# Kernel tuning notes

Measured on AMD Instinct MI355X. Metric: run time of the kernel, lower is better.

## Reference

```python
import jax, jax.numpy as jnp
import numpy as np
import math

HIDDEN = 256

def setup_inputs() -> dict:
    key = jax.random.key(0)
    ks = jax.random.split(key, 4)
    x = jax.random.normal(ks[0], (64, 1024, 32), dtype=jnp.float32)
    Wq = jax.random.normal(ks[1], (32, HIDDEN), dtype=jnp.float32) * (1.0 / math.sqrt(32))
    Wk = jax.random.normal(ks[2], (32, HIDDEN), dtype=jnp.float32) * (1.0 / math.sqrt(32))
    Wv = jax.random.normal(ks[3], (32, HIDDEN), dtype=jnp.float32) * (1.0 / math.sqrt(32))
    bq = jnp.zeros((HIDDEN,), jnp.float32)
    bk = jnp.zeros((HIDDEN,), jnp.float32)
    bv = jnp.zeros((HIDDEN,), jnp.float32)
    return {"x": x, "Wq": Wq, "bq": bq, "Wk": Wk, "bk": bk, "Wv": Wv, "bv": bv}

def reference(x, Wq, bq, Wk, bk, Wv, bv):
    # per-sample single-head attention; softmax FIRST, then divide by sqrt(hidden)
    Q = jnp.einsum('bsi,ih->bsh', x, Wq) + bq  # [B,S,H]
    K = jnp.einsum('bsi,ih->bsh', x, Wk) + bk
    V = jnp.einsum('bsi,ih->bsh', x, Wv) + bv
    scores = jnp.einsum('bqh,bkh->bqk', Q, K)  # [B,S,S]
    attn = jax.nn.softmax(scores, axis=-1) / jnp.sqrt(jnp.float32(Q.shape[-1]))
    Z = jnp.einsum('bqk,bkh->bqh', attn, V)
    return Z
```

## Files before the change

kernel.cpp:

```cpp
#include <hip/hip_runtime.h>
#include <math.h>

#define NB   64
#define SEQ  1024
#define DIN  32
#define HID  256
#define QT   128
#define KT   64
#define NKT  (SEQ/KT)

typedef float        f32x16 __attribute__((ext_vector_type(16)));
typedef short        s16x8  __attribute__((ext_vector_type(8)));
typedef unsigned int u32x4v __attribute__((ext_vector_type(4)));
typedef unsigned int u32x2v __attribute__((ext_vector_type(2)));

#define MFMA32(A,B,C) __builtin_amdgcn_mfma_f32_32x32x16_bf16(A,B,C,0,0,0)

#define SETB(g,p) (((g)*2+(p))*12288)
#define ATS_OFF   49152
#define SMEM_SZ   (ATS_OFF + 4224)

__device__ __forceinline__ unsigned pk_bf16(float lo, float hi) {
  unsigned r;
  asm("v_cvt_pk_bf16_f32 %0, %1, %2" : "=v"(r) : "v"(lo), "v"(hi));
  return r;
}
__device__ __forceinline__ void plswap(unsigned &vdst, unsigned &vsrc) {
  u32x2v r = __builtin_amdgcn_permlane32_swap(vdst, vsrc, false, false);
  vdst = r[0]; vsrc = r[1];
}
__device__ __forceinline__ float cross_max(float v) {
  u32x2v r = __builtin_amdgcn_permlane32_swap(__float_as_uint(v), __float_as_uint(v), false, false);
  return fmaxf(__uint_as_float(r[0]), __uint_as_float(r[1]));
}
__device__ __forceinline__ float cross_add(float v) {
  u32x2v r = __builtin_amdgcn_permlane32_swap(__float_as_uint(v), __float_as_uint(v), false, false);
  return __uint_as_float(r[0]) + __uint_as_float(r[1]);
}
__device__ __forceinline__ s16x8 frag4(unsigned a, unsigned b, unsigned c, unsigned d) {
  u32x4v t; t[0]=a; t[1]=b; t[2]=c; t[3]=d;
  return __builtin_bit_cast(s16x8, t);
}
__device__ __forceinline__ unsigned bf16_hi_bits(float f) {
  unsigned ux = __float_as_uint(f);
  return (ux + 0x7fffu + ((ux >> 16) & 1u)) >> 16;
}

__global__ void precompute_kernel(const float* __restrict__ Wq, const float* __restrict__ Wk,
                                  const float* __restrict__ bq, const float* __restrict__ Wv,
                                  float* __restrict__ ws) {
  const int gid = blockIdx.x * 256 + threadIdx.x;
  if (gid < 1024) {
    int i = gid >> 5, j = gid & 31;
    const float* a  = Wq + j * HID;
    const float* b2 = Wk + i * HID;
    float a0 = 0.f, a1 = 0.f, a2 = 0.f, a3 = 0.f;
    for (int h = 0; h < HID; h += 8) {
      float4 x1 = *(const float4*)(a + h);
      float4 y1 = *(const float4*)(b2 + h);
      float4 x2 = *(const float4*)(a + h + 4);
      float4 y2 = *(const float4*)(b2 + h + 4);
      a0 = fmaf(x1.x, y1.x, a0); a1 = fmaf(x1.y, y1.y, a1);
      a2 = fmaf(x1.z, y1.z, a2); a3 = fmaf(x1.w, y1.w, a3);
      a0 = fmaf(x2.x, y2.x, a0); a1 = fmaf(x2.y, y2.y, a1);
      a2 = fmaf(x2.z, y2.z, a2); a3 = fmaf(x2.w, y2.w, a3);
    }
    ws[gid] = (a0 + a1) + (a2 + a3);
  } else if (gid < 1056) {
    int i2 = gid - 1024;
    const float* b2 = Wk + i2 * HID;
    float acc = 0.f;
    for (int h = 0; h < HID; ++h) acc = fmaf(b2[h], bq[h], acc);
    ws[1024 + i2] = acc;
  } else if (gid < 1056 + HID * 16) {
    int e = gid - 1056;
    int h = e >> 4, d = e & 15;
    ((unsigned*)((char*)ws + 4224))[e] = pk_bf16(Wv[(2*d) * HID + h], Wv[(2*d+1) * HID + h]);
  }
}

__global__ __launch_bounds__(512, 4) void attn_kernel(
    const float* __restrict__ x, const float* __restrict__ ws,
    const float* __restrict__ bv, float* __restrict__ out) {
  __shared__ __align__(16) char smem[SMEM_SZ];
  const int b    = blockIdx.y;
  const int q0   = blockIdx.x * QT;
  const int t    = threadIdx.x;
  const int grp  = t >> 8;
  const int ts   = t & 255;
  const int wid  = t >> 6;
  const int wq   = wid & 3;
  const int lane = t & 63;
  const int w    = lane >> 5;
  const int lq   = lane & 31;
  const float* xb = x + (size_t)b * SEQ * DIN;

  float* ATs = (float*)(smem + ATS_OFF);
  for (int e = t; e < 1056; e += 512) ATs[e] = ws[e];

  {
    const int sb = SETB(grp, 0);
    const int r = ts >> 2, s4 = ts & 3;
    const float* src = xb + (size_t)(grp * KT + r) * DIN + s4 * 8;
    float4 va = *(const float4*)src;
    float4 vb = *(const float4*)(src + 4);
    unsigned h0 = bf16_hi_bits(va.x) | (bf16_hi_bits(va.y) << 16);
    unsigned h1 = bf16_hi_bits(va.z) | (bf16_hi_bits(va.w) << 16);
    unsigned h2 = bf16_hi_bits(vb.x) | (bf16_hi_bits(vb.y) << 16);
    unsigned h3 = bf16_hi_bits(vb.z) | (bf16_hi_bits(vb.w) << 16);
    unsigned l0 = bf16_hi_bits(va.x - __uint_as_float(h0<<16)) | (bf16_hi_bits(va.y - __uint_as_float(h0 & 0xffff0000u)) << 16);
    unsigned l1 = bf16_hi_bits(va.z - __uint_as_float(h1<<16)) | (bf16_hi_bits(va.w - __uint_as_float(h1 & 0xffff0000u)) << 16);
    unsigned l2 = bf16_hi_bits(vb.x - __uint_as_float(h2<<16)) | (bf16_hi_bits(vb.y - __uint_as_float(h2 & 0xffff0000u)) << 16);
    unsigned l3 = bf16_hi_bits(vb.z - __uint_as_float(h3<<16)) | (bf16_hi_bits(vb.w - __uint_as_float(h3 & 0xffff0000u)) << 16);
    int off = r*64 + ((s4 ^ (r & 3)) << 4);
    *(u32x4v*)(smem + sb + off)        = (u32x4v){h0,h1,h2,h3};
    *(u32x4v*)(smem + sb + 4096 + off) = (u32x4v){l0,l1,l2,l3};
    const int ci = ts & 31, cr = (ts >> 5) * 8;
    const float* cs = xb + (size_t)(grp * KT + cr) * DIN + ci;
    float c0=cs[0], c1=cs[DIN], c2=cs[2*DIN], c3=cs[3*DIN];
    float c4=cs[4*DIN], c5=cs[5*DIN], c6=cs[6*DIN], c7=cs[7*DIN];
    unsigned t0 = pk_bf16(c0,c1), t1 = pk_bf16(c2,c3), t2 = pk_bf16(c4,c5), t3 = pk_bf16(c6,c7);
    int toff = sb + 8192 + ci*128 + (((ts>>5) ^ (ci & 7)) << 4);
    *(u32x4v*)(smem + toff) = (u32x4v){t0,t1,t2,t3};
  }
  __syncthreads();

  float g[16];
  {
    float xq[32];
    const float* xrow = xb + (size_t)(q0 + wq*32 + lq) * DIN;
    #pragma unroll
    for (int c = 0; c < 8; ++c) {
      float4 v = *(const float4*)(xrow + c*4);
      xq[c*4+0]=v.x; xq[c*4+1]=v.y; xq[c*4+2]=v.z; xq[c*4+3]=v.w;
    }
    #pragma unroll
    for (int ii = 0; ii < 16; ++ii) {
      const int i = 8*w + 16*(ii>>3) + (ii&7);
      const float* ar = ATs + i*32;
      float acc = ATs[1024 + i];
      #pragma unroll
      for (int j = 0; j < 8; ++j) {
        float4 av = *(const float4*)(ar + j*4);
        acc = fmaf(xq[j*4+0], av.x, acc);
        acc = fmaf(xq[j*4+1], av.y, acc);
        acc = fmaf(xq[j*4+2], av.z, acc);
        acc = fmaf(xq[j*4+3], av.w, acc);
      }
      g[ii] = acc;
    }
  }
  s16x8 G0h, G0l, G1h, G1l;
  {
    unsigned gh[2][4], gl[2][4];
    #pragma unroll
    for (int Ks = 0; Ks < 2; ++Ks)
      #pragma unroll
      for (int d = 0; d < 4; ++d) {
        float ga = g[Ks*8 + 2*d], gb = g[Ks*8 + 2*d + 1];
        unsigned hp = bf16_hi_bits(ga) | (bf16_hi_bits(gb) << 16);
        unsigned lp = bf16_hi_bits(ga - __uint_as_float(hp<<16)) |
                      (bf16_hi_bits(gb - __uint_as_float(hp & 0xffff0000u)) << 16);
        gh[Ks][d] = hp; gl[Ks][d] = lp;
      }
    G0h = frag4(gh[0][0],gh[0][1],gh[0][2],gh[0][3]);
    G0l = frag4(gl[0][0],gl[0][1],gl[0][2],gl[0][3]);
    G1h = frag4(gh[1][0],gh[1][1],gh[1][2],gh[1][3]);
    G1l = frag4(gl[1][0],gl[1][1],gl[1][2],gl[1][3]);
  }

  f32x16 oacc;
  #pragma unroll
  for (int r = 0; r < 16; ++r) oacc[r] = 0.f;
  float m = -INFINITY, l = 0.f;

  for (int j = 0; j < NKT/2; ++j) {
    const bool hn = (j + 1 < NKT/2);
    float4 va, vb;
    float c0=0,c1=0,c2=0,c3=0,c4=0,c5=0,c6=0,c7=0;
    if (hn) {
      const int ktn = 2*(j+1) + grp;
      const int r = ts >> 2, s4 = ts & 3;
      const float* src = xb + (size_t)(ktn*KT + r) * DIN + s4*8;
      va = *(const float4*)src;
      vb = *(const float4*)(src + 4);
      const int ci = ts & 31, cr = (ts >> 5) * 8;
      const float* cs = xb + (size_t)(ktn*KT + cr) * DIN + ci;
      c0=cs[0]; c1=cs[DIN]; c2=cs[2*DIN]; c3=cs[3*DIN];
      c4=cs[4*DIN]; c5=cs[5*DIN]; c6=cs[6*DIN]; c7=cs[7*DIN];
    }

    const int sb = SETB(grp, j & 1);
    const char* bh = smem + sb;
    const char* bl = smem + sb + 4096;
    const int co0 = ((w    ) ^ (lq & 3)) << 4;
    const int co1 = ((w + 2) ^ (lq & 3)) << 4;
    s16x8 ah00 = *(const s16x8*)(bh + lq*64 + co0);
    s16x8 ah01 = *(const s16x8*)(bh + lq*64 + co1);
    s16x8 al00 = *(const s16x8*)(bl + lq*64 + co0);
    s16x8 al01 = *(const s16x8*)(bl + lq*64 + co1);
    s16x8 ah10 = *(const s16x8*)(bh + (32+lq)*64 + co0);
    s16x8 ah11 = *(const s16x8*)(bh + (32+lq)*64 + co1);
    s16x8 al10 = *(const s16x8*)(bl + (32+lq)*64 + co0);
    s16x8 al11 = *(const s16x8*)(bl + (32+lq)*64 + co1);
    f32x16 sa0, sa1;
    #pragma unroll
    for (int r = 0; r < 16; ++r) { sa0[r] = 0.f; sa1[r] = 0.f; }
    sa0 = MFMA32(ah00, G0h, sa0); sa0 = MFMA32(ah00, G0l, sa0); sa0 = MFMA32(al00, G0h, sa0);
    sa0 = MFMA32(ah01, G1h, sa0); sa0 = MFMA32(ah01, G1l, sa0); sa0 = MFMA32(al01, G1h, sa0);
    sa1 = MFMA32(ah10, G0h, sa1); sa1 = MFMA32(ah10, G0l, sa1); sa1 = MFMA32(al10, G0h, sa1);
    sa1 = MFMA32(ah11, G1h, sa1); sa1 = MFMA32(ah11, G1l, sa1); sa1 = MFMA32(al11, G1h, sa1);

    float tm = sa0[0];
    #pragma unroll
    for (int r = 1; r < 16; ++r) tm = fmaxf(tm, sa0[r]);
    #pragma unroll
    for (int r = 0; r < 16; ++r) tm = fmaxf(tm, sa1[r]);
    tm = cross_max(tm);
    float mn = fmaxf(m, tm);
    float alpha = __expf(m - mn);
    m = mn;
    float ps = 0.f;
    #pragma unroll
    for (int r = 0; r < 16; ++r) { float p = __expf(sa0[r] - mn); sa0[r] = p; ps += p; }
    #pragma unroll
    for (int r = 0; r < 16; ++r) { float p = __expf(sa1[r] - mn); sa1[r] = p; ps += p; }
    ps = cross_add(ps);
    l = l * alpha + ps;
    #pragma unroll
    for (int r = 0; r < 16; ++r) oacc[r] *= alpha;

    const char* bt = smem + sb + 8192;
    {
      unsigned u0 = pk_bf16(sa0[0], sa0[1]),  u1 = pk_bf16(sa0[2], sa0[3]);
      unsigned v0 = pk_bf16(sa0[4], sa0[5]),  v1 = pk_bf16(sa0[6], sa0[7]);
      plswap(u0, v0); plswap(u1, v1);
      s16x8 at0 = *(const s16x8*)(bt + lq*128 + (((0 + w) ^ (lq & 7)) << 4));
      oacc = MFMA32(at0, frag4(u0, u1, v0, v1), oacc);

      unsigned u2 = pk_bf16(sa0[8], sa0[9]),   u3 = pk_bf16(sa0[10], sa0[11]);
      unsigned v2 = pk_bf16(sa0[12], sa0[13]), v3 = pk_bf16(sa0[14], sa0[15]);
      plswap(u2, v2); plswap(u3, v3);
      s16x8 at1 = *(const s16x8*)(bt + lq*128 + (((2 + w) ^ (lq & 7)) << 4));
      oacc = MFMA32(at1, frag4(u2, u3, v2, v3), oacc);

      unsigned u4 = pk_bf16(sa1[0], sa1[1]),  u5 = pk_bf16(sa1[2], sa1[3]);
      unsigned v4 = pk_bf16(sa1[4], sa1[5]),  v5 = pk_bf16(sa1[6], sa1[7]);
      plswap(u4, v4); plswap(u5, v5);
      s16x8 at2 = *(const s16x8*)(bt + lq*128 + (((4 + w) ^ (lq & 7)) << 4));
      oacc = MFMA32(at2, frag4(u4, u5, v4, v5), oacc);

      unsigned u6 = pk_bf16(sa1[8], sa1[9]),   u7 = pk_bf16(sa1[10], sa1[11]);
      unsigned v6 = pk_bf16(sa1[12], sa1[13]), v7 = pk_bf16(sa1[14], sa1[15]);
      plswap(u6, v6); plswap(u7, v7);
      s16x8 at3 = *(const s16x8*)(bt + lq*128 + (((6 + w) ^ (lq & 7)) << 4));
      oacc = MFMA32(at3, frag4(u6, u7, v6, v7), oacc);
    }

    if (hn) {
      const int nsb = SETB(grp, (j+1) & 1);
      const int r = ts >> 2, s4 = ts & 3;
      unsigned h0 = bf16_hi_bits(va.x) | (bf16_hi_bits(va.y) << 16);
      unsigned h1 = bf16_hi_bits(va.z) | (bf16_hi_bits(va.w) << 16);
      unsigned h2 = bf16_hi_bits(vb.x) | (bf16_hi_bits(vb.y) << 16);
      unsigned h3 = bf16_hi_bits(vb.z) | (bf16_hi_bits(vb.w) << 16);
      unsigned l0 = bf16_hi_bits(va.x - __uint_as_float(h0<<16)) | (bf16_hi_bits(va.y - __uint_as_float(h0 & 0xffff0000u)) << 16);
      unsigned l1 = bf16_hi_bits(va.z - __uint_as_float(h1<<16)) | (bf16_hi_bits(va.w - __uint_as_float(h1 & 0xffff0000u)) << 16);
      unsigned l2 = bf16_hi_bits(vb.x - __uint_as_float(h2<<16)) | (bf16_hi_bits(vb.y - __uint_as_float(h2 & 0xffff0000u)) << 16);
      unsigned l3 = bf16_hi_bits(vb.z - __uint_as_float(h3<<16)) | (bf16_hi_bits(vb.w - __uint_as_float(h3 & 0xffff0000u)) << 16);
      int off = r*64 + ((s4 ^ (r & 3)) << 4);
      *(u32x4v*)(smem + nsb + off)        = (u32x4v){h0,h1,h2,h3};
      *(u32x4v*)(smem + nsb + 4096 + off) = (u32x4v){l0,l1,l2,l3};
      const int ci = ts & 31;
      unsigned t0 = pk_bf16(c0,c1), t1 = pk_bf16(c2,c3), t2 = pk_bf16(c4,c5), t3 = pk_bf16(c6,c7);
      int toff = nsb + 8192 + ci*128 + (((ts>>5) ^ (ci & 7)) << 4);
      *(u32x4v*)(smem + toff) = (u32x4v){t0,t1,t2,t3};
    }
    __syncthreads();
  }

  {
    float* ms = (float*)(smem + grp*20480 + (((wq<<6) | lane) * 80));
    *(float4*)(ms + 0)  = (float4){oacc[0],  oacc[1],  oacc[2],  oacc[3]};
    *(float4*)(ms + 4)  = (float4){oacc[4],  oacc[5],  oacc[6],  oacc[7]};
    *(float4*)(ms + 8)  = (float4){oacc[8],  oacc[9],  oacc[10], oacc[11]};
    *(float4*)(ms + 12) = (float4){oacc[12], oacc[13], oacc[14], oacc[15]};
    ms[16] = m; ms[17] = l;
    __syncthreads();
    const float* pp = (const float*)(smem + (1-grp)*20480 + (((wq<<6) | lane) * 80));
    float4 p0 = *(const float4*)(pp + 0);
    float4 p1 = *(const float4*)(pp + 4);
    float4 p2 = *(const float4*)(pp + 8);
    float4 p3 = *(const float4*)(pp + 12);
    float pm = pp[16], pl = pp[17];
    float mf = fmaxf(m, pm);
    float as = __expf(m - mf), ap = __expf(pm - mf);
    l = l * as + pl * ap;
    float po[16] = {p0.x,p0.y,p0.z,p0.w, p1.x,p1.y,p1.z,p1.w,
                    p2.x,p2.y,p2.z,p2.w, p3.x,p3.y,p3.z,p3.w};
    #pragma unroll
    for (int r = 0; r < 16; ++r) oacc[r] = oacc[r] * as + po[r] * ap;
    __syncthreads();
  }

  float inv = 1.0f / (16.0f * l);
  #pragma unroll
  for (int r = 0; r < 16; ++r) oacc[r] *= inv;
  s16x8 of0, of1;
  {
    unsigned u0 = pk_bf16(oacc[0], oacc[1]),  u1 = pk_bf16(oacc[2], oacc[3]);
    unsigned v0 = pk_bf16(oacc[4], oacc[5]),  v1 = pk_bf16(oacc[6], oacc[7]);
    plswap(u0, v0); plswap(u1, v1);
    of0 = frag4(u0, u1, v0, v1);
    unsigned u2 = pk_bf16(oacc[8], oacc[9]),   u3 = pk_bf16(oacc[10], oacc[11]);
    unsigned v2 = pk_bf16(oacc[12], oacc[13]), v3 = pk_bf16(oacc[14], oacc[15]);
    plswap(u2, v2); plswap(u3, v3);
    of1 = frag4(u2, u3, v2, v3);
  }
  const char* WvTb = (const char*)ws + 4224;
  float* zb = (float*)(smem + wid * 4224);
  const size_t orow = ((size_t)b * SEQ + q0 + wq*32);
  #pragma unroll 1
  for (int mi = 0; mi < 4; ++mi) {
    const int mt = grp*4 + mi;
    const char* wp = WvTb + (mt*32 + lq)*64 + 16*w;
    s16x8 a0 = *(const s16x8*)wp;
    s16x8 a1 = *(const s16x8*)(wp + 32);
    f32x16 z;
    #pragma unroll
    for (int r = 0; r < 16; ++r) z[r] = 0.f;
    z = MFMA32(a0, of0, z);
    z = MFMA32(a1, of1, z);
    #pragma unroll
    for (int r = 0; r < 16; ++r) {
      int hl = (r&3) + 8*(r>>2) + 4*w;
      zb[hl*33 + lq] = z[r];
    }
    asm volatile("s_waitcnt lgkmcnt(0)" ::: "memory");
    float bvv = bv[mt*32 + lq] * 0.0625f;
    #pragma unroll
    for (int jj = 0; jj < 16; ++jj) {
      int q = w*16 + jj;
      out[(orow + q)*HID + mt*32 + lq] = zb[lq*33 + q] + bvv;
    }
    asm volatile("s_waitcnt lgkmcnt(0)" ::: "memory");
  }
}

extern "C" void kernel_launch(void* const* d_in, const int* in_sizes, int n_in,
                              void* d_out, int out_size, void* d_ws, size_t ws_size,
                              hipStream_t stream) {
  (void)in_sizes; (void)n_in; (void)out_size; (void)ws_size;
  const float* x  = (const float*)d_in[0];
  const float* Wq = (const float*)d_in[1];
  const float* bq = (const float*)d_in[2];
  const float* Wk = (const float*)d_in[3];
  const float* Wv = (const float*)d_in[5];
  const float* bv = (const float*)d_in[6];
  float* out = (float*)d_out;
  float* ws  = (float*)d_ws;

  precompute_kernel<<<24, 256, 0, stream>>>(Wq, Wk, bq, Wv, ws);
  attn_kernel<<<dim3(SEQ/QT, NB), 512, 0, stream>>>(x, ws, bv, out);
}
```

Baseline: 64.96 us.

## Add prepacked fp16 split-precision fast path for attention

Adds a separate pack kernel that converts x into MFMA-fragment-ordered fp16 hi/lo tiles and precomputes G = x·(WqWk^T) rows in split fp16, all written to workspace. A new attention kernel then loads these fragments directly from global memory, with no shared-memory staging, and uses fp16 MFMAs with a 3-term hi/lo split for the scores. The goal is to remove in-kernel conversion and LDS traffic. The cost is an extra kernel launch, a large workspace round-trip, and a grid swizzle. The path is taken only when the workspace is large enough; otherwise the old kernels run.

```diff
diff --git a/kernel.cpp b/kernel.cpp
--- a/kernel.cpp
+++ b/kernel.cpp
@@ -11,10 +11,18 @@
 
 typedef float        f32x16 __attribute__((ext_vector_type(16)));
 typedef short        s16x8  __attribute__((ext_vector_type(8)));
+typedef _Float16     f16x8  __attribute__((ext_vector_type(8)));
 typedef unsigned int u32x4v __attribute__((ext_vector_type(4)));
 typedef unsigned int u32x2v __attribute__((ext_vector_type(2)));
 
-#define MFMA32(A,B,C) __builtin_amdgcn_mfma_f32_32x32x16_bf16(A,B,C,0,0,0)
+#define MFMA32(A,B,C)  __builtin_amdgcn_mfma_f32_32x32x16_bf16(A,B,C,0,0,0)
+#define MFMA32H(A,B,C) __builtin_amdgcn_mfma_f32_32x32x16_f16(A,B,C,0,0,0)
+
+#define OFF_WVT  4224
+#define OFF_G    24576
+#define OFF_A    (OFF_G + 64*1024*128)
+#define OFF_T    (OFF_A + 64*16*8192)
+#define WS_NEED  ((size_t)OFF_T + 64*16*4096)
 
 #define SETB(g,p) (((g)*2+(p))*12288)
 #define ATS_OFF   49152
@@ -25,6 +33,9 @@
   asm("v_cvt_pk_bf16_f32 %0, %1, %2" : "=v"(r) : "v"(lo), "v"(hi));
   return r;
 }
+__device__ __forceinline__ unsigned pkh(float a, float b) {
+  return __builtin_bit_cast(unsigned, __builtin_amdgcn_cvt_pkrtz(a, b));
+}
 __device__ __forceinline__ void plswap(unsigned &vdst, unsigned &vsrc) {
   u32x2v r = __builtin_amdgcn_permlane32_swap(vdst, vsrc, false, false);
   vdst = r[0]; vsrc = r[1];
@@ -41,10 +52,271 @@
   u32x4v t; t[0]=a; t[1]=b; t[2]=c; t[3]=d;
   return __builtin_bit_cast(s16x8, t);
 }
+__device__ __forceinline__ f16x8 frag4h(unsigned a, unsigned b, unsigned c, unsigned d) {
+  u32x4v t; t[0]=a; t[1]=b; t[2]=c; t[3]=d;
+  return __builtin_bit_cast(f16x8, t);
+}
+__device__ __forceinline__ f16x8 ldh(const void* p) {
+  return __builtin_bit_cast(f16x8, *(const u32x4v*)p);
+}
 __device__ __forceinline__ unsigned bf16_hi_bits(float f) {
   unsigned ux = __float_as_uint(f);
   return (ux + 0x7fffu + ((ux >> 16) & 1u)) >> 16;
 }
+__device__ __forceinline__ unsigned pack_h2(float a, float b) {
+  _Float16 ha = (_Float16)a, hb = (_Float16)b;
+  return (unsigned)__builtin_bit_cast(unsigned short, ha) |
+         ((unsigned)__builtin_bit_cast(unsigned short, hb) << 16);
+}
+
+
+__global__ void prep1_kernel(const float* __restrict__ Wq, const float* __restrict__ Wk,
+                             const float* __restrict__ bq, const float* __restrict__ Wv,
+                             float* __restrict__ ws) {
+  const int gid = blockIdx.x * 256 + threadIdx.x;
+  if (gid < 1024) {
+    int i = gid >> 5, j = gid & 31;
+    const float* a  = Wq + j * HID;
+    const float* b2 = Wk + i * HID;
+    float a0=0.f,a1=0.f,a2=0.f,a3=0.f;
+    for (int h = 0; h < HID; h += 8) {
+      float4 x1 = *(const float4*)(a + h),  y1 = *(const float4*)(b2 + h);
+      float4 x2 = *(const float4*)(a + h+4), y2 = *(const float4*)(b2 + h+4);
+      a0 = fmaf(x1.x,y1.x,a0); a1 = fmaf(x1.y,y1.y,a1);
+      a2 = fmaf(x1.z,y1.z,a2); a3 = fmaf(x1.w,y1.w,a3);
+      a0 = fmaf(x2.x,y2.x,a0); a1 = fmaf(x2.y,y2.y,a1);
+      a2 = fmaf(x2.z,y2.z,a2); a3 = fmaf(x2.w,y2.w,a3);
+    }
+    ws[gid] = (a0+a1)+(a2+a3);
+  } else if (gid < 1056) {
+    int i2 = gid - 1024;
+    const float* b2 = Wk + i2 * HID;
+    float acc = 0.f;
+    for (int h = 0; h < HID; ++h) acc = fmaf(b2[h], bq[h], acc);
+    ws[1024 + i2] = acc;
+  } else if (gid < 1056 + HID*16) {
+    int e = gid - 1056;
+    int h = e >> 4, d = e & 15;
+    ((unsigned*)((char*)ws + OFF_WVT))[e] = pkh(Wv[(2*d)*HID + h], Wv[(2*d+1)*HID + h]);
+  }
+}
+
+__global__ void pack_kernel(const float* __restrict__ x, char* __restrict__ ws) {
+  const int gid = blockIdx.x * 256 + threadIdx.x;
+  if (gid < 262144) {
+    const int l = gid & 63, f = (gid>>6)&3, kt = (gid>>8)&15, b = gid>>12;
+    const int w = l>>5, lq = l&31;
+    const int row = ((f&2)?32:0) + lq;
+    const int d0  = ((f&1)?16:0) + 8*w;
+    const float* s = x + ((size_t)(b*SEQ + kt*KT + row))*DIN + d0;
+    float4 v0 = *(const float4*)s, v1 = *(const float4*)(s+4);
+    float vv[8] = {v0.x,v0.y,v0.z,v0.w, v1.x,v1.y,v1.z,v1.w};
+    unsigned hi[4], lo[4];
+    #pragma unroll
+    for (int j = 0; j < 4; ++j) {
+      float a = vv[2*j], c = vv[2*j+1];
+      _Float16 ha = (_Float16)a, hb = (_Float16)c;
+      hi[j] = (unsigned)__builtin_bit_cast(unsigned short, ha) |
+              ((unsigned)__builtin_bit_cast(unsigned short, hb) << 16);
+      lo[j] = pack_h2(a - (float)ha, c - (float)hb);
+    }
+    char* dst = ws + OFF_A + (size_t)(b*16 + kt)*8192 + f*1024 + l*16;
+    *(u32x4v*)dst          = (u32x4v){hi[0],hi[1],hi[2],hi[3]};
+    *(u32x4v*)(dst + 4096) = (u32x4v){lo[0],lo[1],lo[2],lo[3]};
+  } else if (gid < 524288) {
+    const int e = gid - 262144;
+    const int l = e & 63, f = (e>>6)&3, kt = (e>>8)&15, b = e>>12;
+    const int w = l>>5, lq = l&31;
+    const int k0 = 16*f + 8*w;
+    const float* s = x + ((size_t)(b*SEQ + kt*KT + k0))*DIN + lq;
+    unsigned hi[4];
+    #pragma unroll
+    for (int j = 0; j < 4; ++j)
+      hi[j] = pack_h2(s[(2*j)*DIN], s[(2*j+1)*DIN]);
+    char* dst = ws + OFF_T + (size_t)(b*16 + kt)*4096 + f*1024 + l*16;
+    *(u32x4v*)dst = (u32x4v){hi[0],hi[1],hi[2],hi[3]};
+  } else if (gid < 524288 + 65536) {
+    const int e = gid - 524288;
+    const int q = e & 1023, b = e >> 10;
+    const float* xr = x + (size_t)(b*SEQ + q)*DIN;
+    float xq[32];
+    #pragma unroll
+    for (int c = 0; c < 8; ++c) {
+      float4 v = *(const float4*)(xr + 4*c);
+      xq[4*c]=v.x; xq[4*c+1]=v.y; xq[4*c+2]=v.z; xq[4*c+3]=v.w;
+    }
+    const float* AT = (const float*)ws;
+    unsigned hw[16], lw[16];
+    #pragma unroll 4
+    for (int p = 0; p < 16; ++p) {
+      float g2[2];
+      #pragma unroll
+      for (int s2 = 0; s2 < 2; ++s2) {
+        int i = 2*p + s2;
+        float acc = AT[1024 + i];
+        const float* ar = AT + i*32;
+        #pragma unroll
+        for (int j = 0; j < 32; j += 4) {
+          float4 av = *(const float4*)(ar + j);
+          acc = fmaf(xq[j],av.x,acc); acc = fmaf(xq[j+1],av.y,acc);
+          acc = fmaf(xq[j+2],av.z,acc); acc = fmaf(xq[j+3],av.w,acc);
+        }
+        g2[s2] = acc;
+      }
+      _Float16 ha = (_Float16)g2[0], hb = (_Float16)g2[1];
+      hw[p] = (unsigned)__builtin_bit_cast(unsigned short, ha) |
+              ((unsigned)__builtin_bit_cast(unsigned short, hb) << 16);
+      lw[p] = pack_h2(g2[0] - (float)ha, g2[1] - (float)hb);
+    }
+    char* dst = ws + OFF_G + (size_t)(b*SEQ + q)*128;
+    *(u32x4v*)(dst +  0) = (u32x4v){hw[0],hw[1],hw[2],hw[3]};
+    *(u32x4v*)(dst + 16) = (u32x4v){hw[4],hw[5],hw[6],hw[7]};
+    *(u32x4v*)(dst + 32) = (u32x4v){hw[8],hw[9],hw[10],hw[11]};
+    *(u32x4v*)(dst + 48) = (u32x4v){hw[12],hw[13],hw[14],hw[15]};
+    *(u32x4v*)(dst + 64) = (u32x4v){lw[0],lw[1],lw[2],lw[3]};
+    *(u32x4v*)(dst + 80) = (u32x4v){lw[4],lw[5],lw[6],lw[7]};
+    *(u32x4v*)(dst + 96) = (u32x4v){lw[8],lw[9],lw[10],lw[11]};
+    *(u32x4v*)(dst +112) = (u32x4v){lw[12],lw[13],lw[14],lw[15]};
+  }
+}
+
+__global__ __launch_bounds__(256) void attn_fast(
+    const float* __restrict__ x, const char* __restrict__ ws,
+    const float* __restrict__ bv, float* __restrict__ out) {
+  __shared__ __align__(16) float zbs[4*1056];
+  const int bid = blockIdx.x;
+  const int vid = (bid & 7) * 64 + (bid >> 3);
+  const int b   = vid >> 3;
+  const int q0  = (vid & 7) * QT;
+  const int t = threadIdx.x;
+  const int wid = t>>6, lane = t&63, w = lane>>5, lq = lane&31;
+  (void)x;
+
+  const char* gp = ws + OFF_G + (size_t)(b*SEQ + q0 + wid*32 + lq)*128;
+  f16x8 G0h = ldh(gp + 16*w);
+  f16x8 G1h = ldh(gp + 32 + 16*w);
+  f16x8 G0l = ldh(gp + 64 + 16*w);
+  f16x8 G1l = ldh(gp + 96 + 16*w);
+
+  f32x16 oacc;
+  #pragma unroll
+  for (int r = 0; r < 16; ++r) oacc[r] = 0.f;
+  float m = -INFINITY, l = 0.f;
+
+  const char* Ab = ws + OFF_A + (size_t)(b*16)*8192;
+  const char* Tb = ws + OFF_T + (size_t)(b*16)*4096;
+  const int lo16 = lane*16;
+
+  #pragma unroll
+  for (int kt = 0; kt < NKT; ++kt) {
+    const char* A = Ab + kt*8192;
+    const char* T = Tb + kt*4096;
+    f16x8 ah0 = ldh(A + 0*1024 + lo16);
+    f16x8 ah1 = ldh(A + 1*1024 + lo16);
+    f16x8 ah2 = ldh(A + 2*1024 + lo16);
+    f16x8 ah3 = ldh(A + 3*1024 + lo16);
+    f16x8 al0 = ldh(A + 4096 + 0*1024 + lo16);
+    f16x8 al1 = ldh(A + 4096 + 1*1024 + lo16);
+    f16x8 al2 = ldh(A + 4096 + 2*1024 + lo16);
+    f16x8 al3 = ldh(A + 4096 + 3*1024 + lo16);
+    f16x8 at0 = ldh(T + 0*1024 + lo16);
+    f16x8 at1 = ldh(T + 1*1024 + lo16);
+    f16x8 at2 = ldh(T + 2*1024 + lo16);
+    f16x8 at3 = ldh(T + 3*1024 + lo16);
+
+    f32x16 sa0, sa1;
+    #pragma unroll
+    for (int r = 0; r < 16; ++r) { sa0[r] = 0.f; sa1[r] = 0.f; }
+    sa0 = MFMA32H(ah0, G0h, sa0); sa0 = MFMA32H(ah0, G0l, sa0); sa0 = MFMA32H(al0, G0h, sa0);
+    sa0 = MFMA32H(ah1, G1h, sa0); sa0 = MFMA32H(ah1, G1l, sa0); sa0 = MFMA32H(al1, G1h, sa0);
+    sa1 = MFMA32H(ah2, G0h, sa1); sa1 = MFMA32H(ah2, G0l, sa1); sa1 = MFMA32H(al2, G0h, sa1);
+    sa1 = MFMA32H(ah3, G1h, sa1); sa1 = MFMA32H(ah3, G1l, sa1); sa1 = MFMA32H(al3, G1h, sa1);
+
+    float tm = sa0[0];
+    #pragma unroll
+    for (int r = 1; r < 16; ++r) tm = fmaxf(tm, sa0[r]);
+    #pragma unroll
+    for (int r = 0; r < 16; ++r) tm = fmaxf(tm, sa1[r]);
+    tm = cross_max(tm);
+    float mn = fmaxf(m, tm);
+    float alpha = __expf(m - mn);
+    m = mn;
+    float ps = 0.f;
+    #pragma unroll
+    for (int r = 0; r < 16; ++r) { float p = __expf(sa0[r] - mn); sa0[r] = p; ps += p; }
+    #pragma unroll
+    for (int r = 0; r < 16; ++r) { float p = __expf(sa1[r] - mn); sa1[r] = p; ps += p; }
+    ps = cross_add(ps);
+    l = l * alpha + ps;
+    #pragma unroll
+    for (int r = 0; r < 16; ++r) oacc[r] *= alpha;
+
+    {
+      unsigned u0 = pkh(sa0[0], sa0[1]),  u1 = pkh(sa0[2], sa0[3]);
+      unsigned v0 = pkh(sa0[4], sa0[5]),  v1 = pkh(sa0[6], sa0[7]);
+      plswap(u0, v0); plswap(u1, v1);
+      oacc = MFMA32H(at0, frag4h(u0, u1, v0, v1), oacc);
+
+      unsigned u2 = pkh(sa0[8], sa0[9]),   u3 = pkh(sa0[10], sa0[11]);
+      unsigned v2 = pkh(sa0[12], sa0[13]), v3 = pkh(sa0[14], sa0[15]);
+      plswap(u2, v2); plswap(u3, v3);
+      oacc = MFMA32H(at1, frag4h(u2, u3, v2, v3), oacc);
+
+      unsigned u4 = pkh(sa1[0], sa1[1]),  u5 = pkh(sa1[2], sa1[3]);
+      unsigned v4 = pkh(sa1[4], sa1[5]),  v5 = pkh(sa1[6], sa1[7]);
+      plswap(u4, v4); plswap(u5, v5);
+      oacc = MFMA32H(at2, frag4h(u4, u5, v4, v5), oacc);
+
+      unsigned u6 = pkh(sa1[8], sa1[9]),   u7 = pkh(sa1[10], sa1[11]);
+      unsigned v6 = pkh(sa1[12], sa1[13]), v7 = pkh(sa1[14], sa1[15]);
+      plswap(u6, v6); plswap(u7, v7);
+      oacc = MFMA32H(at3, frag4h(u6, u7, v6, v7), oacc);
+    }
+  }
+
+  float inv = 1.0f / (16.0f * l);
+  #pragma unroll
+  for (int r = 0; r < 16; ++r) oacc[r] *= inv;
+  f16x8 of0, of1;
+  {
+    unsigned u0 = pkh(oacc[0], oacc[1]),  u1 = pkh(oacc[2], oacc[3]);
+    unsigned v0 = pkh(oacc[4], oacc[5]),  v1 = pkh(oacc[6], oacc[7]);
+    plswap(u0, v0); plswap(u1, v1);
+    of0 = frag4h(u0, u1, v0, v1);
+    unsigned u2 = pkh(oacc[8], oacc[9]),   u3 = pkh(oacc[10], oacc[11]);
+    unsigned v2 = pkh(oacc[12], oacc[13]), v3 = pkh(oacc[14], oacc[15]);
+    plswap(u2, v2); plswap(u3, v3);
+    of1 = frag4h(u2, u3, v2, v3);
+  }
+  const char* WvTb = ws + OFF_WVT;
+  float* zb = zbs + wid * 1056;
+  const size_t orow = ((size_t)b * SEQ + q0 + wid*32);
+  #pragma unroll 1
+  for (int mt = 0; mt < 8; ++mt) {
+    const char* wp = WvTb + (mt*32 + lq)*64 + 16*w;
+    f16x8 a0 = ldh(wp);
+    f16x8 a1 = ldh(wp + 32);
+    f32x16 z;
+    #pragma unroll
+    for (int r = 0; r < 16; ++r) z[r] = 0.f;
+    z = MFMA32H(a0, of0, z);
+    z = MFMA32H(a1, of1, z);
+    #pragma unroll
+    for (int r = 0; r < 16; ++r) {
+      int hl = (r&3) + 8*(r>>2) + 4*w;
+      zb[hl*33 + lq] = z[r];
+    }
+    asm volatile("s_waitcnt lgkmcnt(0)" ::: "memory");
+    float bvv = bv[mt*32 + lq] * 0.0625f;
+    #pragma unroll
+    for (int jj = 0; jj < 16; ++jj) {
+      int q = w*16 + jj;
+      out[(orow + q)*HID + mt*32 + lq] = zb[lq*33 + q] + bvv;
+    }
+    asm volatile("s_waitcnt lgkmcnt(0)" ::: "memory");
+  }
+}
+
 
 __global__ void precompute_kernel(const float* __restrict__ Wq, const float* __restrict__ Wk,
                                   const float* __restrict__ bq, const float* __restrict__ Wv,
@@ -54,28 +326,26 @@
     int i = gid >> 5, j = gid & 31;
     const float* a  = Wq + j * HID;
     const float* b2 = Wk + i * HID;
-    float a0 = 0.f, a1 = 0.f, a2 = 0.f, a3 = 0.f;
+    float a0=0.f,a1=0.f,a2=0.f,a3=0.f;
     for (int h = 0; h < HID; h += 8) {
-      float4 x1 = *(const float4*)(a + h);
-      float4 y1 = *(const float4*)(b2 + h);
-      float4 x2 = *(const float4*)(a + h + 4);
-      float4 y2 = *(const float4*)(b2 + h + 4);
-      a0 = fmaf(x1.x, y1.x, a0); a1 = fmaf(x1.y, y1.y, a1);
-      a2 = fmaf(x1.z, y1.z, a2); a3 = fmaf(x1.w, y1.w, a3);
-      a0 = fmaf(x2.x, y2.x, a0); a1 = fmaf(x2.y, y2.y, a1);
-      a2 = fmaf(x2.z, y2.z, a2); a3 = fmaf(x2.w, y2.w, a3);
-    }
-    ws[gid] = (a0 + a1) + (a2 + a3);
+      float4 x1 = *(const float4*)(a + h),  y1 = *(const float4*)(b2 + h);
+      float4 x2 = *(const float4*)(a + h+4), y2 = *(const float4*)(b2 + h+4);
+      a0 = fmaf(x1.x,y1.x,a0); a1 = fmaf(x1.y,y1.y,a1);
+      a2 = fmaf(x1.z,y1.z,a2); a3 = fmaf(x1.w,y1.w,a3);
+      a0 = fmaf(x2.x,y2.x,a0); a1 = fmaf(x2.y,y2.y,a1);
+      a2 = fmaf(x2.z,y2.z,a2); a3 = fmaf(x2.w,y2.w,a3);
+    }
+    ws[gid] = (a0+a1)+(a2+a3);
   } else if (gid < 1056) {
     int i2 = gid - 1024;
     const float* b2 = Wk + i2 * HID;
     float acc = 0.f;
     for (int h = 0; h < HID; ++h) acc = fmaf(b2[h], bq[h], acc);
     ws[1024 + i2] = acc;
-  } else if (gid < 1056 + HID * 16) {
+  } else if (gid < 1056 + HID*16) {
     int e = gid - 1056;
     int h = e >> 4, d = e & 15;
-    ((unsigned*)((char*)ws + 4224))[e] = pk_bf16(Wv[(2*d) * HID + h], Wv[(2*d+1) * HID + h]);
+    ((unsigned*)((char*)ws + 4224))[e] = pk_bf16(Wv[(2*d)*HID + h], Wv[(2*d+1)*HID + h]);
   }
 }
 
@@ -350,7 +620,7 @@
 extern "C" void kernel_launch(void* const* d_in, const int* in_sizes, int n_in,
                               void* d_out, int out_size, void* d_ws, size_t ws_size,
                               hipStream_t stream) {
-  (void)in_sizes; (void)n_in; (void)out_size; (void)ws_size;
+  (void)in_sizes; (void)n_in; (void)out_size;
   const float* x  = (const float*)d_in[0];
   const float* Wq = (const float*)d_in[1];
   const float* bq = (const float*)d_in[2];
@@ -360,6 +630,12 @@
   float* out = (float*)d_out;
   float* ws  = (float*)d_ws;
 
-  precompute_kernel<<<24, 256, 0, stream>>>(Wq, Wk, bq, Wv, ws);
-  attn_kernel<<<dim3(SEQ/QT, NB), 512, 0, stream>>>(x, ws, bv, out);
-}
+  if (ws_size >= WS_NEED) {
+    prep1_kernel<<<24, 256, 0, stream>>>(Wq, Wk, bq, Wv, ws);
+    pack_kernel<<<2304, 256, 0, stream>>>(x, (char*)ws);
+    attn_fast<<<512, 256, 0, stream>>>(x, (const char*)ws, bv, out);
+  } else {
+    precompute_kernel<<<24, 256, 0, stream>>>(Wq, Wk, bq, Wv, ws);
+    attn_kernel<<<dim3(SEQ/QT, NB), 512, 0, stream>>>(x, ws, bv, out);
+  }
+}
```

Result: slower. 72.99 us (+12.3%).
